# Kernel optimization log

Measured on AMD Instinct MI355X. Metric: run time of the kernel, lower is better.

Reference implementation:

```python
import jax, jax.numpy as jnp
import numpy as np
import math

H = 16  # heads
EPS = 1e-5

def _gelu_tanh(x):
    c = math.sqrt(2.0 / math.pi)
    return 0.5 * x * (1.0 + jnp.tanh(c * (x + 0.044715 * x * x * x)))

def _layernorm(x, g, b):
    mu = jnp.mean(x, axis=-1, keepdims=True)
    var = jnp.mean((x - mu) ** 2, axis=-1, keepdims=True)
    return (x - mu) / jnp.sqrt(var + EPS) * g + b


def setup_inputs() -> dict:
    key = jax.random.key(0)
    ks = jax.random.split(key, 16)
    B, S, D, F = 8, 1024, 1024, 4096
    s = 1.0 / math.sqrt(D)
    inp = {
        "x": jax.random.normal(ks[0], (B, S, D), jnp.float32),
        "mask": jax.random.randint(ks[1], (B, 1, S, S), 0, 2, jnp.int32),
        "Wq": jax.random.normal(ks[2], (D, D), jnp.float32) * s,
        "bq": jnp.zeros((D,), jnp.float32),
        "Wk": jax.random.normal(ks[3], (D, D), jnp.float32) * s,
        "bk": jnp.zeros((D,), jnp.float32),
        "Wv": jax.random.normal(ks[4], (D, D), jnp.float32) * s,
        "bv": jnp.zeros((D,), jnp.float32),
        "Wo": jax.random.normal(ks[5], (D, D), jnp.float32) * s,
        "bo": jnp.zeros((D,), jnp.float32),
        "W1": jax.random.normal(ks[6], (D, F), jnp.float32) * s,
        "b1": jnp.zeros((F,), jnp.float32),
        "W2": jax.random.normal(ks[7], (F, D), jnp.float32) * (1.0 / math.sqrt(F)),
        "b2": jnp.zeros((D,), jnp.float32),
        "ln1_g": jnp.ones((D,), jnp.float32),
        "ln1_b": jnp.zeros((D,), jnp.float32),
        "ln2_g": jnp.ones((D,), jnp.float32),
        "ln2_b": jnp.zeros((D,), jnp.float32),
    }
    return inp


def reference(x, mask, Wq, bq, Wk, bk, Wv, bv, Wo, bo, W1, b1, W2, b2,
              ln1_g, ln1_b, ln2_g, ln2_b):
    B, S, D = x.shape
    dk = D // H

    # --- sublayer 1: pre-LN multi-head attention + residual ---
    y = _layernorm(x, ln1_g, ln1_b)
    q = (y @ Wq + bq).reshape(B, S, H, dk).transpose(0, 2, 1, 3)  # [B,H,S,dk]
    k = (y @ Wk + bk).reshape(B, S, H, dk).transpose(0, 2, 1, 3)
    v = (y @ Wv + bv).reshape(B, S, H, dk).transpose(0, 2, 1, 3)

    scores = jnp.einsum('bhqd,bhkd->bhqk', q, k) / jnp.sqrt(jnp.float32(dk))
    scores = jnp.where(mask == 0, jnp.float32(-1e9), scores)
    p = jax.nn.softmax(scores, axis=-1)
    a = jnp.einsum('bhqk,bhkd->bhqd', p, v)
    a = a.transpose(0, 2, 1, 3).reshape(B, S, D)
    x = x + (a @ Wo + bo)

    # --- sublayer 2: pre-LN GELU FFN + residual ---
    y = _layernorm(x, ln2_g, ln2_b)
    h = _gelu_tanh(y @ W1 + b1)
    return x + (h @ W2 + b2)
```

## Files before the change

kernel.cpp:

```cpp
#include <hip/hip_runtime.h>
#include <math.h>

typedef unsigned short u16;
typedef short bf16x8 __attribute__((ext_vector_type(8)));
typedef float f32x4 __attribute__((ext_vector_type(4)));

#define DEV static __device__ __forceinline__

DEV float bf2f(u16 u) {
  union { unsigned int i; float f; } v; v.i = ((unsigned int)u) << 16; return v.f;
}
DEV u16 f2bf(float f) {
  union { float f; unsigned int i; } v; v.f = f;
  unsigned int x = v.i;
  return (u16)((x + 0x7FFFu + ((x >> 16) & 1u)) >> 16);
}

DEV void gload16(const void* gsrc, void* ldst) {
  __builtin_amdgcn_global_load_lds(
      (__attribute__((address_space(1))) void*)gsrc,
      (__attribute__((address_space(3))) void*)ldst, 16, 0, 0);
}

DEV f32x4 mfma16(bf16x8 a, bf16x8 b, f32x4 c) {
  return __builtin_amdgcn_mfma_f32_16x16x32_bf16(a, b, c, 0, 0, 0);
}

template <int EPI, int WF32>
__global__ __launch_bounds__(256)
void gemm_nt(const u16* __restrict__ A, const u16* __restrict__ Bt,
             const float* __restrict__ bias, const float* __restrict__ res,
             void* __restrict__ Cv, int M, int N, int K) {
  __shared__ __align__(16) u16 Asm[128 * 64];
  __shared__ __align__(16) u16 Bsm[128 * 64];
  const int ntn = N >> 7;
  const int tm = blockIdx.x / ntn, tn = blockIdx.x % ntn;
  const int tid = threadIdx.x;
  const int wave = tid >> 6, lane = tid & 63;
  const int wm = wave >> 1, wn = wave & 1;
  const int lg = lane >> 4, lr = lane & 15;

  f32x4 acc[4][4];
#pragma unroll
  for (int i = 0; i < 4; ++i)
#pragma unroll
    for (int j = 0; j < 4; ++j)
#pragma unroll
      for (int r = 0; r < 4; ++r) acc[i][j][r] = 0.f;

  const char* Ab = (const char*)(A + (size_t)tm * 128 * K);
  const char* Bb = (const char*)(Bt + (size_t)tn * 128 * K);
  char* As = (char*)Asm;
  char* Bs = (char*)Bsm;
  const size_t rowbytes = (size_t)K * 2;

  for (int kb = 0; kb < K; kb += 64) {
#pragma unroll
    for (int c = 0; c < 4; ++c) {
      const int chunk = wave * 4 + c;
      const int p = chunk * 1024 + lane * 16;
      const int f = p ^ (((p >> 7) & 7) << 4);
      const int row = f >> 7, colb = f & 127;
      gload16(Ab + (size_t)row * rowbytes + (size_t)kb * 2 + colb, As + chunk * 1024);
      gload16(Bb + (size_t)row * rowbytes + (size_t)kb * 2 + colb, Bs + chunk * 1024);
    }
    __syncthreads();
#pragma unroll
    for (int ks = 0; ks < 2; ++ks) {
      bf16x8 af[4], bfr[4];
#pragma unroll
      for (int fm = 0; fm < 4; ++fm) {
        const int row = wm * 64 + fm * 16 + lr;
        const int addr = ((row << 7) | (ks * 64 + lg * 16)) ^ ((row & 7) << 4);
        af[fm] = *(const bf16x8*)(As + addr);
      }
#pragma unroll
      for (int fn = 0; fn < 4; ++fn) {
        const int row = wn * 64 + fn * 16 + lr;
        const int addr = ((row << 7) | (ks * 64 + lg * 16)) ^ ((row & 7) << 4);
        bfr[fn] = *(const bf16x8*)(Bs + addr);
      }
#pragma unroll
      for (int fm = 0; fm < 4; ++fm)
#pragma unroll
        for (int fn = 0; fn < 4; ++fn)
          acc[fm][fn] = mfma16(af[fm], bfr[fn], acc[fm][fn]);
    }
    __syncthreads();
  }

#pragma unroll
  for (int fm = 0; fm < 4; ++fm)
#pragma unroll
    for (int fn = 0; fn < 4; ++fn) {
      const int col = tn * 128 + wn * 64 + fn * 16 + lr;
      const float bc = bias[col];
#pragma unroll
      for (int r = 0; r < 4; ++r) {
        const int row = tm * 128 + wm * 64 + fm * 16 + lg * 4 + r;
        float vv = acc[fm][fn][r] + bc;
        if (EPI == 1) {
          const float u = vv;
          const float t = tanhf(0.7978845608028654f * (u + 0.044715f * u * u * u));
          vv = 0.5f * u * (1.0f + t);
        } else if (EPI == 2) {
          vv += res[(size_t)row * N + col];
        } else if (EPI == 3) {
          vv *= 0.180336880111112f;
        }
        if (WF32)
          ((float*)Cv)[(size_t)row * N + col] = vv;
        else
          ((u16*)Cv)[(size_t)row * N + col] = f2bf(vv);
      }
    }
}

__global__ __launch_bounds__(256)
void attn_kernel(const u16* __restrict__ Q, const u16* __restrict__ Km,
                 const u16* __restrict__ Vt, const u16* __restrict__ maskT4,
                 u16* __restrict__ O) {
  const int bid = (int)blockIdx.x;
  const int swz = (bid & 7) * 256 + (bid >> 3);
  const int qb = swz & 15;
  const int bh = swz >> 4;
  const int b = bh >> 4, h = bh & 15;
  const int wave = threadIdx.x >> 6, lane = threadIdx.x & 63;
  const int lg = lane >> 4, lr = lane & 15;
  __shared__ __align__(16) u16 Ksm[2][64 * 64];
  __shared__ __align__(16) u16 Vsm[2][64 * 64];
  __shared__ __align__(16) u16 Pl[4][1024];
  char* Pb = (char*)&Pl[wave][0];
  const int swx = (lr & 7) << 4;

  const int q0 = qb * 64 + wave * 16;
  const u16* Qp = Q + ((size_t)(b * 1024 + q0)) * 1024 + h * 64;
  bf16x8 qf[2];
#pragma unroll
  for (int ks = 0; ks < 2; ++ks)
    qf[ks] = *(const bf16x8*)(Qp + (size_t)lr * 1024 + ks * 32 + lg * 8);

  float l = 0.f;
  f32x4 accO[4];
#pragma unroll
  for (int fc = 0; fc < 4; ++fc)
#pragma unroll
    for (int r = 0; r < 4; ++r) accO[fc][r] = 0.f;

  const char* Kg = (const char*)(Km + (size_t)(b * 1024) * 1024 + h * 64);
  const char* Vg = (const char*)(Vt + (size_t)(bh * 64) * 1024);
  const ushort4* Mb0 = (const ushort4*)maskT4 + (size_t)b * 256 * 1024 + q0 + lr;

#define STAGE_KV(T, BUF)                                                      \
  {                                                                           \
    const int kb_ = (T) * 64;                                                 \
    _Pragma("unroll")                                                         \
    for (int c = 0; c < 2; ++c) {                                             \
      const int chunk = wave * 2 + c;                                         \
      const int p = chunk * 1024 + lane * 16;                                 \
      const int f = p ^ (((p >> 7) & 7) << 4);                                \
      const int row = f >> 7, colb = f & 127;                                 \
      gload16(Kg + (size_t)(kb_ + row) * 2048 + colb,                         \
              (char*)Ksm[BUF] + chunk * 1024);                                \
      gload16(Vg + (size_t)row * 2048 + (size_t)kb_ * 2 + colb,               \
              (char*)Vsm[BUF] + chunk * 1024);                                \
    }                                                                         \
  }

  STAGE_KV(0, 0);
  __syncthreads();

  for (int t = 0; t < 16; ++t) {
    const int cb = t & 1;
    if (t < 15) STAGE_KV(t + 1, cb ^ 1);

    ushort4 mv[4];
#pragma unroll
    for (int fc = 0; fc < 4; ++fc)
      mv[fc] = Mb0[(size_t)(t * 16 + fc * 4 + lg) * 1024];

    f32x4 ts[4];
#pragma unroll
    for (int fc = 0; fc < 4; ++fc)
#pragma unroll
      for (int r = 0; r < 4; ++r) ts[fc][r] = 0.f;
    __builtin_amdgcn_s_setprio(1);
#pragma unroll
    for (int ks = 0; ks < 2; ++ks)
#pragma unroll
      for (int fc = 0; fc < 4; ++fc) {
        const int row = fc * 16 + lr;
        const int ad = ((row << 7) | (ks * 64 + lg * 16)) ^ ((row & 7) << 4);
        const bf16x8 kfr = *(const bf16x8*)((const char*)Ksm[cb] + ad);
        ts[fc] = mfma16(kfr, qf[ks], ts[fc]);
      }
    __builtin_amdgcn_s_setprio(0);

#pragma unroll
    for (int fc = 0; fc < 4; ++fc) {
      const float p0 = exp2f(ts[fc][0] + bf2f(mv[fc].x));
      const float p1 = exp2f(ts[fc][1] + bf2f(mv[fc].y));
      const float p2 = exp2f(ts[fc][2] + bf2f(mv[fc].z));
      const float p3 = exp2f(ts[fc][3] + bf2f(mv[fc].w));
      l += (p0 + p1) + (p2 + p3);
      unsigned int w0, w1;
      asm("v_cvt_pk_bf16_f32 %0, %1, %2" : "=v"(w0) : "v"(p0), "v"(p1));
      asm("v_cvt_pk_bf16_f32 %0, %1, %2" : "=v"(w1) : "v"(p2), "v"(p3));
      const int base = lr * 128 + fc * 32 + lg * 8;
      *(unsigned int*)(Pb + ((base + 0) ^ swx)) = w0;
      *(unsigned int*)(Pb + ((base + 4) ^ swx)) = w1;
    }

    __builtin_amdgcn_s_setprio(1);
#pragma unroll
    for (int ks = 0; ks < 2; ++ks) {
      const int ad = (lr * 128 + ks * 64 + lg * 16) ^ swx;
      const bf16x8 pa = *(const bf16x8*)(Pb + ad);
#pragma unroll
      for (int fc = 0; fc < 4; ++fc) {
        const int row = fc * 16 + lr;
        const int vad = ((row << 7) | (ks * 64 + lg * 16)) ^ ((row & 7) << 4);
        const bf16x8 vfr = *(const bf16x8*)((const char*)Vsm[cb] + vad);
        accO[fc] = mfma16(pa, vfr, accO[fc]);
      }
    }
    __builtin_amdgcn_s_setprio(0);

    __syncthreads();
  }

  l += __shfl_xor(l, 16);
  l += __shfl_xor(l, 32);
  float linv[4];
#pragma unroll
  for (int r = 0; r < 4; ++r) linv[r] = 1.0f / __shfl(l, lg * 4 + r);

  u16* Op = O + ((size_t)(b * 1024 + q0)) * 1024 + h * 64;
#pragma unroll
  for (int fc = 0; fc < 4; ++fc)
#pragma unroll
    for (int r = 0; r < 4; ++r)
      Op[(size_t)(lg * 4 + r) * 1024 + fc * 16 + lr] = f2bf(accO[fc][r] * linv[r]);
#undef STAGE_KV
}

__global__ __launch_bounds__(256)
void transpose_cast(const float* __restrict__ in, u16* __restrict__ out, int R, int C) {
  __shared__ u16 t[64][65];
  const int ctiles = C >> 6;
  const int bx = blockIdx.x % ctiles, by = blockIdx.x / ctiles;
  const int tc = threadIdx.x & 63, t4 = threadIdx.x >> 6;
#pragma unroll
  for (int i = 0; i < 16; ++i) {
    const int r = i * 4 + t4;
    t[r][tc] = f2bf(in[(size_t)(by * 64 + r) * C + bx * 64 + tc]);
  }
  __syncthreads();
#pragma unroll
  for (int i = 0; i < 16; ++i) {
    const int r = i * 4 + t4;
    out[(size_t)(bx * 64 + r) * R + by * 64 + tc] = t[tc][r];
  }
}

__global__ __launch_bounds__(256)
void transpose_v_kernel(const u16* __restrict__ v, u16* __restrict__ vt) {
  const int st = blockIdx.x & 15, bh = blockIdx.x >> 4;
  __shared__ u16 t[64][65];
  const int tc = threadIdx.x & 63, t4 = threadIdx.x >> 6;
  const u16* src = v + ((size_t)((bh >> 4) * 1024 + st * 64)) * 1024 + (bh & 15) * 64;
#pragma unroll
  for (int i = 0; i < 16; ++i) {
    const int r = i * 4 + t4;
    t[r][tc] = src[(size_t)r * 1024 + tc];
  }
  __syncthreads();
  u16* dst = vt + (size_t)bh * 64 * 1024 + st * 64;
#pragma unroll
  for (int i = 0; i < 16; ++i) {
    const int r = i * 4 + t4;
    dst[(size_t)r * 1024 + tc] = t[tc][r];
  }
}

__global__ __launch_bounds__(256)
void mask_t_kernel(const int* __restrict__ mask, u16* __restrict__ mt) {
  const int bt = blockIdx.x;
  const int b = bt >> 8;
  const int kt = (bt >> 4) & 15;
  const int qt = bt & 15;
  __shared__ u16 t[64][65];
  const int tc = threadIdx.x & 63, t4 = threadIdx.x >> 6;
  const u16 neg = f2bf(-1.442695040888963e9f);
  const int* src = mask + ((size_t)b * 1024 + qt * 64) * 1024 + kt * 64;
#pragma unroll
  for (int i = 0; i < 16; ++i) {
    const int q = i * 4 + t4;
    t[q][tc] = src[(size_t)q * 1024 + tc] ? (u16)0 : neg;
  }
  __syncthreads();
  ushort4* dst = (ushort4*)mt + ((size_t)b * 256 + kt * 16) * 1024 + qt * 64;
#pragma unroll
  for (int i = 0; i < 4; ++i) {
    const int kg = i * 4 + t4;
    ushort4 o;
    o.x = t[tc][kg * 4 + 0];
    o.y = t[tc][kg * 4 + 1];
    o.z = t[tc][kg * 4 + 2];
    o.w = t[tc][kg * 4 + 3];
    dst[(size_t)kg * 1024 + tc] = o;
  }
}

__global__ __launch_bounds__(256)
void ln_kernel(const float* __restrict__ x, const float* __restrict__ g,
               const float* __restrict__ bb, u16* __restrict__ y) {
  const int row = blockIdx.x, tid = threadIdx.x;
  const float4 v = ((const float4*)(x + (size_t)row * 1024))[tid];
  float s = v.x + v.y + v.z + v.w;
  float ss = v.x * v.x + v.y * v.y + v.z * v.z + v.w * v.w;
#pragma unroll
  for (int mk = 1; mk < 64; mk <<= 1) {
    s += __shfl_xor(s, mk);
    ss += __shfl_xor(ss, mk);
  }
  __shared__ float sa[4], sq[4];
  const int wave = tid >> 6, lane = tid & 63;
  if (lane == 0) { sa[wave] = s; sq[wave] = ss; }
  __syncthreads();
  s = sa[0] + sa[1] + sa[2] + sa[3];
  ss = sq[0] + sq[1] + sq[2] + sq[3];
  const float mu = s * 0.0009765625f;
  const float var = ss * 0.0009765625f - mu * mu;
  const float inv = rsqrtf(var + 1e-5f);
  const float4 gg = ((const float4*)g)[tid];
  const float4 bv = ((const float4*)bb)[tid];
  ushort4 o;
  o.x = f2bf((v.x - mu) * inv * gg.x + bv.x);
  o.y = f2bf((v.y - mu) * inv * gg.y + bv.y);
  o.z = f2bf((v.z - mu) * inv * gg.z + bv.z);
  o.w = f2bf((v.w - mu) * inv * gg.w + bv.w);
  *(ushort4*)(y + (size_t)row * 1024 + tid * 4) = o;
}

extern "C" void kernel_launch(void* const* d_in, const int* in_sizes, int n_in,
                              void* d_out, int out_size, void* d_ws, size_t ws_size,
                              hipStream_t stream) {
  (void)in_sizes; (void)n_in; (void)out_size; (void)ws_size;
  const float* x  = (const float*)d_in[0];
  const int* mask = (const int*)d_in[1];
  const float* Wq = (const float*)d_in[2];  const float* bq = (const float*)d_in[3];
  const float* Wk = (const float*)d_in[4];  const float* bk = (const float*)d_in[5];
  const float* Wv = (const float*)d_in[6];  const float* bv = (const float*)d_in[7];
  const float* Wo = (const float*)d_in[8];  const float* bo = (const float*)d_in[9];
  const float* W1 = (const float*)d_in[10]; const float* b1 = (const float*)d_in[11];
  const float* W2 = (const float*)d_in[12]; const float* b2 = (const float*)d_in[13];
  const float* g1 = (const float*)d_in[14]; const float* be1 = (const float*)d_in[15];
  const float* g2 = (const float*)d_in[16]; const float* be2 = (const float*)d_in[17];

  float* out = (float*)d_out;

  u16* ws = (u16*)d_ws;
  const size_t M1 = (size_t)1024 * 1024;
  u16* y    = ws;
  u16* q    = ws + 8 * M1;
  u16* kbuf = ws + 16 * M1;
  u16* vbuf = ws + 24 * M1;
  u16* vt   = ws + 32 * M1;
  u16* hbuf = ws + 8 * M1;
  u16* wqt  = ws + 40 * M1;
  u16* wkt  = ws + 41 * M1;
  u16* wvt  = ws + 42 * M1;
  u16* wot  = ws + 43 * M1;
  u16* w1t  = ws + 44 * M1;
  u16* w2t  = ws + 48 * M1;
  u16* maskT4 = y;

  dim3 blk(256);
  transpose_cast<<<256, blk, 0, stream>>>(Wq, wqt, 1024, 1024);
  transpose_cast<<<256, blk, 0, stream>>>(Wk, wkt, 1024, 1024);
  transpose_cast<<<256, blk, 0, stream>>>(Wv, wvt, 1024, 1024);
  transpose_cast<<<256, blk, 0, stream>>>(Wo, wot, 1024, 1024);
  transpose_cast<<<1024, blk, 0, stream>>>(W1, w1t, 1024, 4096);
  transpose_cast<<<1024, blk, 0, stream>>>(W2, w2t, 4096, 1024);
  ln_kernel<<<8192, blk, 0, stream>>>(x, g1, be1, y);
  gemm_nt<3, 0><<<512, blk, 0, stream>>>(y, wqt, bq, nullptr, q, 8192, 1024, 1024);
  gemm_nt<0, 0><<<512, blk, 0, stream>>>(y, wkt, bk, nullptr, kbuf, 8192, 1024, 1024);
  gemm_nt<0, 0><<<512, blk, 0, stream>>>(y, wvt, bv, nullptr, vbuf, 8192, 1024, 1024);
  transpose_v_kernel<<<2048, blk, 0, stream>>>(vbuf, vt);
  mask_t_kernel<<<2048, blk, 0, stream>>>(mask, maskT4);
  attn_kernel<<<2048, blk, 0, stream>>>(q, kbuf, vt, maskT4, vbuf);
  gemm_nt<2, 1><<<512, blk, 0, stream>>>(vbuf, wot, bo, x, out, 8192, 1024, 1024);
  ln_kernel<<<8192, blk, 0, stream>>>(out, g2, be2, y);
  gemm_nt<1, 0><<<2048, blk, 0, stream>>>(y, w1t, b1, nullptr, hbuf, 8192, 4096, 1024);
  gemm_nt<2, 1><<<512, blk, 0, stream>>>(hbuf, w2t, b2, out, out, 8192, 1024, 4096);
}
```

Before: 453.0 us.

## Replace GEMM with 8-wave double-buffered pipelined kernel using larger tiles

Replaces the 256-thread 128x128 single-buffered GEMM with a 512-thread kernel that uses 256xBN tiles (BN = 128 or 256). It double-buffers A and B in LDS with interleaved global-to-LDS loads, explicit vmcnt waits and barriers, and raises MFMA priority with setprio. Workgroups are remapped across XCDs for L2 locality. The aim is to hide load latency and raise operand reuse per LDS byte. In exchange it uses up to 128KB of LDS per workgroup and hand-counted waitcnt values that must match the issued loads exactly.

After: 419.8 us. 1.08x faster.

```diff
diff --git a/kernel.cpp b/kernel.cpp
--- a/kernel.cpp
+++ b/kernel.cpp
@@ -26,79 +26,160 @@
   return __builtin_amdgcn_mfma_f32_16x16x32_bf16(a, b, c, 0, 0, 0);
 }
 
-template <int EPI, int WF32>
-__global__ __launch_bounds__(256)
-void gemm_nt(const u16* __restrict__ A, const u16* __restrict__ Bt,
-             const float* __restrict__ bias, const float* __restrict__ res,
-             void* __restrict__ Cv, int M, int N, int K) {
-  __shared__ __align__(16) u16 Asm[128 * 64];
-  __shared__ __align__(16) u16 Bsm[128 * 64];
-  const int ntn = N >> 7;
-  const int tm = blockIdx.x / ntn, tn = blockIdx.x % ntn;
+template <int EPI, int WF32, int NFR>
+__global__ __launch_bounds__(512, 2)
+void gemm8(const u16* __restrict__ A, const u16* __restrict__ Bt,
+           const float* __restrict__ bias, const float* __restrict__ res,
+           void* __restrict__ Cv, int M, int N, int K) {
+  constexpr int BN = NFR * 64;
+  constexpr int HB = NFR * 4096;
+  __shared__ __align__(16) char Alds[4 * 16384];
+  __shared__ __align__(16) char Blds[4 * HB];
+
+  const int ntn = N / BN;
+  const int nwg = gridDim.x;
+  const int cpx = nwg >> 3;
+  const int bid = (int)blockIdx.x;
+  const int swb = (bid & 7) * cpx + (bid >> 3);
+  const int tm = swb / ntn, tn = swb % ntn;
+
   const int tid = threadIdx.x;
   const int wave = tid >> 6, lane = tid & 63;
-  const int wm = wave >> 1, wn = wave & 1;
+  const int wm = wave >> 2, wn = wave & 3;
   const int lg = lane >> 4, lr = lane & 15;
-
-  f32x4 acc[4][4];
-#pragma unroll
-  for (int i = 0; i < 4; ++i)
-#pragma unroll
-    for (int j = 0; j < 4; ++j)
-#pragma unroll
-      for (int r = 0; r < 4; ++r) acc[i][j][r] = 0.f;
-
-  const char* Ab = (const char*)(A + (size_t)tm * 128 * K);
-  const char* Bb = (const char*)(Bt + (size_t)tn * 128 * K);
-  char* As = (char*)Asm;
-  char* Bs = (char*)Bsm;
-  const size_t rowbytes = (size_t)K * 2;
-
-  for (int kb = 0; kb < K; kb += 64) {
-#pragma unroll
-    for (int c = 0; c < 4; ++c) {
-      const int chunk = wave * 4 + c;
-      const int p = chunk * 1024 + lane * 16;
-      const int f = p ^ (((p >> 7) & 7) << 4);
-      const int row = f >> 7, colb = f & 127;
-      gload16(Ab + (size_t)row * rowbytes + (size_t)kb * 2 + colb, As + chunk * 1024);
-      gload16(Bb + (size_t)row * rowbytes + (size_t)kb * 2 + colb, Bs + chunk * 1024);
-    }
-    __syncthreads();
-#pragma unroll
-    for (int ks = 0; ks < 2; ++ks) {
-      bf16x8 af[4], bfr[4];
-#pragma unroll
-      for (int fm = 0; fm < 4; ++fm) {
-        const int row = wm * 64 + fm * 16 + lr;
-        const int addr = ((row << 7) | (ks * 64 + lg * 16)) ^ ((row & 7) << 4);
-        af[fm] = *(const bf16x8*)(As + addr);
-      }
-#pragma unroll
-      for (int fn = 0; fn < 4; ++fn) {
-        const int row = wn * 64 + fn * 16 + lr;
-        const int addr = ((row << 7) | (ks * 64 + lg * 16)) ^ ((row & 7) << 4);
-        bfr[fn] = *(const bf16x8*)(Bs + addr);
-      }
-#pragma unroll
-      for (int fm = 0; fm < 4; ++fm)
-#pragma unroll
-        for (int fn = 0; fn < 4; ++fn)
-          acc[fm][fn] = mfma16(af[fm], bfr[fn], acc[fm][fn]);
-    }
-    __syncthreads();
-  }
-
-#pragma unroll
-  for (int fm = 0; fm < 4; ++fm)
-#pragma unroll
-    for (int fn = 0; fn < 4; ++fn) {
-      const int col = tn * 128 + wn * 64 + fn * 16 + lr;
+  const int swx = (lr & 7) << 4;
+
+  f32x4 acc[8][NFR];
+#pragma unroll
+  for (int m = 0; m < 8; ++m)
+#pragma unroll
+    for (int n = 0; n < NFR; ++n)
+#pragma unroll
+      for (int r = 0; r < 4; ++r) acc[m][n][r] = 0.f;
+
+  const size_t rowb = (size_t)K * 2;
+  const char* Ab = (const char*)A + (size_t)tm * 256 * rowb;
+  const char* Bb = (const char*)Bt + (size_t)tn * BN * rowb;
+
+  int rowS[2], colS[2];
+#pragma unroll
+  for (int rr = 0; rr < 2; ++rr) {
+    const int p = rr * 8192 + tid * 16;
+    const int f = p ^ (((p >> 7) & 7) << 4);
+    rowS[rr] = f >> 7; colS[rr] = f & 127;
+  }
+
+  const int NT = K >> 6;
+
+#define SA(T, H)                                                              \
+  do {                                                                        \
+    char* d_ = Alds + ((((T) & 1) * 2 + (H)) << 14);                          \
+    _Pragma("unroll")                                                         \
+    for (int r_ = 0; r_ < 2; ++r_)                                            \
+      gload16(Ab + (size_t)((H) * 128 + rowS[r_]) * rowb + (size_t)(T) * 128  \
+                  + colS[r_],                                                 \
+              d_ + r_ * 8192 + wave * 1024);                                  \
+  } while (0)
+
+#define SB(T, H)                                                              \
+  do {                                                                        \
+    char* d_ = Blds + ((((T) & 1) * 2 + (H)) * HB);                           \
+    _Pragma("unroll")                                                         \
+    for (int r_ = 0; r_ < NFR / 2; ++r_)                                      \
+      gload16(Bb + (size_t)((H) * (BN / 2) + rowS[r_]) * rowb                 \
+                  + (size_t)(T) * 128 + colS[r_],                             \
+              d_ + r_ * 8192 + wave * 1024);                                  \
+  } while (0)
+
+#define PHASE(SS, Q, STG, DOVM)                                               \
+  {                                                                           \
+    if ((Q) == 0) {                                                           \
+      _Pragma("unroll")                                                       \
+      for (int n_ = 0; n_ < NFR; ++n_) {                                      \
+        const int g_ = n_ * 4 + wn;                                           \
+        const char* bs_ = Blds + ((SS) * 2 + g_ / (NFR * 2)) * HB;            \
+        const int rb_ = (g_ % (NFR * 2)) * 16 + lr;                           \
+        _Pragma("unroll")                                                     \
+        for (int k_ = 0; k_ < 2; ++k_)                                        \
+          bfr[n_][k_] =                                                       \
+              *(const bf16x8*)(bs_ + ((rb_ * 128 + k_ * 64 + lg * 16) ^ swx));\
+      }                                                                       \
+    }                                                                         \
+    bf16x8 af_[2][2];                                                         \
+    {                                                                         \
+      const char* as_ = Alds + (((SS) * 2 + ((Q) >> 1)) << 14);               \
+      _Pragma("unroll")                                                       \
+      for (int j_ = 0; j_ < 2; ++j_) {                                        \
+        const int ra_ = ((4 * (Q) + 2 * j_ + wm) & 7) * 16 + lr;              \
+        _Pragma("unroll")                                                     \
+        for (int k_ = 0; k_ < 2; ++k_)                                        \
+          af_[j_][k_] =                                                       \
+              *(const bf16x8*)(as_ + ((ra_ * 128 + k_ * 64 + lg * 16) ^ swx));\
+      }                                                                       \
+    }                                                                         \
+    STG;                                                                      \
+    if ((DOVM) == 1) {                                                        \
+      if (NFR == 4) asm volatile("s_waitcnt vmcnt(6)" ::: "memory");          \
+      else          asm volatile("s_waitcnt vmcnt(4)" ::: "memory");          \
+    } else if ((DOVM) == 2) {                                                 \
+      asm volatile("s_waitcnt vmcnt(0)" ::: "memory");                        \
+    }                                                                         \
+    asm volatile("s_barrier" ::: "memory");                                   \
+    __builtin_amdgcn_s_setprio(1);                                            \
+    _Pragma("unroll")                                                         \
+    for (int j_ = 0; j_ < 2; ++j_)                                            \
+      _Pragma("unroll")                                                       \
+      for (int n_ = 0; n_ < NFR; ++n_)                                        \
+        _Pragma("unroll")                                                     \
+        for (int k_ = 0; k_ < 2; ++k_)                                        \
+          acc[2 * (Q) + j_][n_] =                                             \
+              mfma16(af_[j_][k_], bfr[n_][k_], acc[2 * (Q) + j_][n_]);        \
+    __builtin_amdgcn_s_setprio(0);                                            \
+    asm volatile("s_barrier" ::: "memory");                                   \
+  }
+
+  SA(0, 0); SA(0, 1); SB(0, 0); SB(0, 1); SA(1, 0); SB(1, 0); SB(1, 1);
+  asm volatile("s_waitcnt vmcnt(0)" ::: "memory");
+  asm volatile("s_barrier" ::: "memory");
+
+  bf16x8 bfr[NFR][2];
+  const int NIT = NT >> 1;
+  for (int it = 0; it < NIT - 1; ++it) {
+    const int T0 = 2 * it;
+    PHASE(0, 0, SA(T0 + 1, 1), 0)
+    PHASE(0, 1, SB(T0 + 2, 0), 0)
+    PHASE(0, 2, SA(T0 + 2, 0), 0)
+    PHASE(0, 3, SB(T0 + 2, 1), 1)
+    PHASE(1, 0, SA(T0 + 2, 1), 0)
+    PHASE(1, 1, SB(T0 + 3, 0), 0)
+    PHASE(1, 2, SB(T0 + 3, 1), 0)
+    PHASE(1, 3, SA(T0 + 3, 0), 1)
+  }
+  {
+    const int T0 = NT - 2;
+    PHASE(0, 0, SA(T0 + 1, 1), 0)
+    PHASE(0, 1, ((void)0), 0)
+    PHASE(0, 2, ((void)0), 0)
+    PHASE(0, 3, ((void)0), 2)
+    PHASE(1, 0, ((void)0), 0)
+    PHASE(1, 1, ((void)0), 0)
+    PHASE(1, 2, ((void)0), 0)
+    PHASE(1, 3, ((void)0), 0)
+  }
+#undef SA
+#undef SB
+#undef PHASE
+
+#pragma unroll
+  for (int m = 0; m < 8; ++m)
+#pragma unroll
+    for (int n = 0; n < NFR; ++n) {
+      const int col = tn * BN + (n * 4 + wn) * 16 + lr;
       const float bc = bias[col];
 #pragma unroll
       for (int r = 0; r < 4; ++r) {
-        const int row = tm * 128 + wm * 64 + fm * 16 + lg * 4 + r;
-        float vv = acc[fm][fn][r] + bc;
+        const int row = tm * 256 + (2 * m + wm) * 16 + lg * 4 + r;
+        float vv = acc[m][n][r] + bc;
         if (EPI == 1) {
           const float u = vv;
           const float t = tanhf(0.7978845608028654f * (u + 0.044715f * u * u * u));
@@ -377,6 +458,7 @@
   u16* maskT4 = y;
 
   dim3 blk(256);
+  dim3 blk8(512);
   transpose_cast<<<256, blk, 0, stream>>>(Wq, wqt, 1024, 1024);
   transpose_cast<<<256, blk, 0, stream>>>(Wk, wkt, 1024, 1024);
   transpose_cast<<<256, blk, 0, stream>>>(Wv, wvt, 1024, 1024);
@@ -384,14 +466,14 @@
   transpose_cast<<<1024, blk, 0, stream>>>(W1, w1t, 1024, 4096);
   transpose_cast<<<1024, blk, 0, stream>>>(W2, w2t, 4096, 1024);
   ln_kernel<<<8192, blk, 0, stream>>>(x, g1, be1, y);
-  gemm_nt<3, 0><<<512, blk, 0, stream>>>(y, wqt, bq, nullptr, q, 8192, 1024, 1024);
-  gemm_nt<0, 0><<<512, blk, 0, stream>>>(y, wkt, bk, nullptr, kbuf, 8192, 1024, 1024);
-  gemm_nt<0, 0><<<512, blk, 0, stream>>>(y, wvt, bv, nullptr, vbuf, 8192, 1024, 1024);
+  gemm8<3, 0, 2><<<256, blk8, 0, stream>>>(y, wqt, bq, nullptr, q, 8192, 1024, 1024);
+  gemm8<0, 0, 2><<<256, blk8, 0, stream>>>(y, wkt, bk, nullptr, kbuf, 8192, 1024, 1024);
+  gemm8<0, 0, 2><<<256, blk8, 0, stream>>>(y, wvt, bv, nullptr, vbuf, 8192, 1024, 1024);
   transpose_v_kernel<<<2048, blk, 0, stream>>>(vbuf, vt);
   mask_t_kernel<<<2048, blk, 0, stream>>>(mask, maskT4);
   attn_kernel<<<2048, blk, 0, stream>>>(q, kbuf, vt, maskT4, vbuf);
-  gemm_nt<2, 1><<<512, blk, 0, stream>>>(vbuf, wot, bo, x, out, 8192, 1024, 1024);
+  gemm8<2, 1, 2><<<256, blk8, 0, stream>>>(vbuf, wot, bo, x, out, 8192, 1024, 1024);
   ln_kernel<<<8192, blk, 0, stream>>>(out, g2, be2, y);
-  gemm_nt<1, 0><<<2048, blk, 0, stream>>>(y, w1t, b1, nullptr, hbuf, 8192, 4096, 1024);
-  gemm_nt<2, 1><<<512, blk, 0, stream>>>(hbuf, w2t, b2, out, out, 8192, 1024, 4096);
-}
+  gemm8<1, 0, 4><<<512, blk8, 0, stream>>>(y, w1t, b1, nullptr, hbuf, 8192, 4096, 1024);
+  gemm8<2, 1, 2><<<256, blk8, 0, stream>>>(hbuf, w2t, b2, out, out, 8192, 1024, 4096);
+}
```
